# Optimization experiments

Measured on AMD Instinct MI355X. Metric: run time of the kernel, lower is better.

## Reference

```python
import jax, jax.numpy as jnp
import numpy as np

B, N, E, H = 4, 8192, 256, 8
EXP = 4  # params['num_layers'] -> MLP expansion
HID = EXP * E
EPS = 1e-5


def _layernorm(x, w, b):
    mu = jnp.mean(x, axis=-1, keepdims=True)
    var = jnp.mean(jnp.square(x - mu), axis=-1, keepdims=True)
    return (x - mu) * jax.lax.rsqrt(var + EPS) * w + b


def _mish(x):
    return x * jnp.tanh(jax.nn.softplus(x))


def setup_inputs() -> dict:
    key = jax.random.key(0)
    ks = jax.random.split(key, 12)
    s = 0.02
    return {
        "x": jax.random.normal(ks[0], (B, N, E), dtype=jnp.float32),
        "ln1_w": jnp.ones((E,), jnp.float32),
        "ln1_b": jnp.zeros((E,), jnp.float32),
        "Wq": jax.random.normal(ks[1], (E, E), jnp.float32) * s,
        "bq": jnp.zeros((E,), jnp.float32),
        "Wk": jax.random.normal(ks[2], (E, E), jnp.float32) * s,
        "bk": jnp.zeros((E,), jnp.float32),
        "Wv": jax.random.normal(ks[3], (E, E), jnp.float32) * s,
        "bv": jnp.zeros((E,), jnp.float32),
        "Wp": jax.random.normal(ks[4], (E, E), jnp.float32) * s,
        "bp": jnp.zeros((E,), jnp.float32),
        "ln2_w": jnp.ones((E,), jnp.float32),
        "ln2_b": jnp.zeros((E,), jnp.float32),
        "W1": jax.random.normal(ks[5], (HID, E), jnp.float32) * s,
        "b1": jnp.zeros((HID,), jnp.float32),
        "W2": jax.random.normal(ks[6], (E, HID), jnp.float32) * s,
        "b2": jnp.zeros((E,), jnp.float32),
    }


def _msa(x, Wq, bq, Wk, bk, Wv, bv, Wp, bp):
    b, n, e = x.shape
    d = n // H  # sequence-chunk per head (faithful to source rearrange)
    q = (x @ Wq.T + bq).reshape(b, H, d, e)
    k = (x @ Wk.T + bk).reshape(b, H, d, e)
    v = (x @ Wv.T + bv).reshape(b, H, d, e)
    scale = jnp.sqrt(jnp.float32(E))
    energy = jnp.einsum('bhie,bhke->bhik', q, k)  # (b,H,d,d)
    att = jax.nn.softmax(energy, axis=3) / scale
    o = jnp.einsum('bhik,bhke->bhie', att, v).reshape(b, n, e)
    return o @ Wp.T + bp


def reference(x, ln1_w, ln1_b, Wq, bq, Wk, bk, Wv, bv, Wp, bp,
              ln2_w, ln2_b, W1, b1, W2, b2):
    # pre-LN attention block + residual
    x1 = _msa(_layernorm(x, ln1_w, ln1_b), Wq, bq, Wk, bk, Wv, bv, Wp, bp) + x
    # pre-LN MLP (Mish after both linears, per source) + residual
    h = _layernorm(x1, ln2_w, ln2_b)
    h = _mish(h @ W1.T + b1)
    h = _mish(h @ W2.T + b2)
    return h + x1
```

## Files before the change

kernel.cpp:

```cpp
#include <hip/hip_runtime.h>

typedef float  f32x4  __attribute__((ext_vector_type(4)));
typedef float  f4v    __attribute__((ext_vector_type(4)));
typedef __bf16 bf16x8 __attribute__((ext_vector_type(8)));
typedef __bf16 bf16x4 __attribute__((ext_vector_type(4)));
typedef unsigned short ushort_t;

#define AS1 __attribute__((address_space(1)))
#define AS3 __attribute__((address_space(3)))

static __device__ __forceinline__ void gload_lds16(const void* g, void* l) {
  __builtin_amdgcn_global_load_lds((const AS1 void*)g, (AS3 void*)l, 16, 0, 0);
}

static __device__ __forceinline__ float mishf(float x) {
  float t = __expf(x);
  float u = t * (t + 2.f);
  float y = x * __fdividef(u, u + 2.f);
  return (x > 15.f) ? x : y;
}

__global__ __launch_bounds__(256) void packw(
    const float* __restrict__ Wq, const float* __restrict__ Wk,
    const float* __restrict__ Wv, const float* __restrict__ Wp,
    const float* __restrict__ W1, const float* __restrict__ W2,
    __bf16* __restrict__ out)
{
  const int t = blockIdx.x * 256 + threadIdx.x;
  const int e0 = t * 8;
  int rel, K; const float* src;
  if      (e0 < 196608) { rel = e0;          K = 256;  src = nullptr; }
  else if (e0 < 262144) { rel = e0 - 196608; K = 256;  src = Wp; }
  else if (e0 < 524288) { rel = e0 - 262144; K = 256;  src = W1; }
  else                  { rel = e0 - 524288; K = 1024; src = W2; }
  const int percb = (K >> 8) * 8192;
  const int cb = rel / percb;  const int r1 = rel % percb;
  const int c  = r1 / 8192;    const int r2 = r1 % 8192;
  const int u  = r2 / 1024;    const int r3 = r2 % 1024;
  const int n  = r3 / 512;     const int l  = (r3 % 512) >> 3;
  const int col = cb * 32 + n * 16 + (l & 15);
  const int k   = c * 256 + u * 32 + ((l >> 4) << 3);
  const float* sp;
  if (e0 < 196608) {
    const float* qkvsrc = (col < 256) ? Wq : (col < 512 ? Wk : Wv);
    sp = qkvsrc + (size_t)(col & 255) * 256 + k;
  } else {
    sp = src + (size_t)col * K + k;
  }
  const f4v a = *(const f4v*)(sp);
  const f4v b = *(const f4v*)(sp + 4);
  bf16x8 o;
  #pragma unroll
  for (int j = 0; j < 4; ++j) { o[j] = (__bf16)a[j]; o[4 + j] = (__bf16)b[j]; }
  *(bf16x8*)(out + e0) = o;
}

__global__ void packb(const float* __restrict__ a, const float* __restrict__ b,
                      const float* __restrict__ c, float* __restrict__ o) {
  int i = threadIdx.x;
  o[i] = (i < 256) ? a[i] : (i < 512 ? b[i - 256] : c[i - 512]);
}

__global__ __launch_bounds__(256) void ln_rows(
    const float* __restrict__ X, const float* __restrict__ g,
    const float* __restrict__ b, __bf16* __restrict__ Y)
{
  const int l = threadIdx.x & 63;
  const size_t row = (size_t)blockIdx.x * 4 + (threadIdx.x >> 6);
  const f4v x = *(const f4v*)(X + row * 256 + l * 4);
  float s = x[0] + x[1] + x[2] + x[3];
  float q = x[0]*x[0] + x[1]*x[1] + x[2]*x[2] + x[3]*x[3];
  #pragma unroll
  for (int d = 1; d < 64; d <<= 1) { s += __shfl_xor(s, d); q += __shfl_xor(q, d); }
  const float mu = s * (1.f / 256.f);
  const float rs = rsqrtf(q * (1.f / 256.f) - mu * mu + 1e-5f);
  const f4v gv = *(const f4v*)(g + l * 4);
  const f4v bv = *(const f4v*)(b + l * 4);
  bf16x4 o;
  #pragma unroll
  for (int j = 0; j < 4; ++j) o[j] = (__bf16)((x[j] - mu) * rs * gv[j] + bv[j]);
  *(bf16x4*)(Y + row * 256 + l * 4) = o;
}

template<int BM, int NT, int KC, int ACT, int RES, int OUTBF>
__global__ __launch_bounds__(512, 2) void bgemm(
    const __bf16* __restrict__ A, const __bf16* __restrict__ Wg,
    const float* __restrict__ bias, const float* __restrict__ res,
    void* __restrict__ out, int ldo)
{
  constexpr int K  = KC * 256;
  constexpr int MR = BM / 16;
  __shared__ __bf16 Ab[BM * 256];
  const int tid = threadIdx.x, l = tid & 63, w = tid >> 6;
  constexpr int nwg = (32768 / BM) * NT;
  const int wg = (blockIdx.x & 7) * (nwg / 8) + (blockIdx.x >> 3);
  const int mt = wg / NT, nt = wg % NT;
  const int row0 = mt * BM;
  const int col0 = nt * 256 + w * 32;
  const int cb = nt * 8 + w;

  auto stageA = [&](int c) {
    #pragma unroll
    for (int j = 0; j < BM / 16; ++j) {
      const int s = j * 512 + tid;
      const int r = s >> 5, q = s & 31;
      gload_lds16(A + (size_t)(row0 + r) * K + c * 256 + ((q ^ (r & 7)) << 3),
                  &Ab[s << 3]);
    }
  };

  bf16x8 bf[2][8];
  auto loadB = [&](int c) {
    const __bf16* wp = Wg + (size_t)(cb * KC + c) * 8192;
    #pragma unroll
    for (int u = 0; u < 8; ++u)
      #pragma unroll
      for (int n = 0; n < 2; ++n)
        bf[n][u] = *(const bf16x8*)(wp + (((u << 1) | n) * 64 + l) * 8);
  };

  f32x4 acc[MR][2] = {};

  stageA(0); loadB(0);
  asm volatile("s_waitcnt vmcnt(0)" ::: "memory");
  __builtin_amdgcn_s_barrier();

  for (int c = 0;;) {
    #pragma unroll
    for (int u = 0; u < 8; ++u) {
      bf16x8 af[MR];
      #pragma unroll
      for (int m = 0; m < MR; ++m) {
        const int r = m * 16 + (l & 15);
        const int q = ((u << 2) | (l >> 4)) ^ (r & 7);
        af[m] = *(const bf16x8*)&Ab[((r << 5) | q) << 3];
      }
      #pragma unroll
      for (int m = 0; m < MR; ++m) {
        acc[m][0] = __builtin_amdgcn_mfma_f32_16x16x32_bf16(af[m], bf[0][u], acc[m][0], 0, 0, 0);
        acc[m][1] = __builtin_amdgcn_mfma_f32_16x16x32_bf16(af[m], bf[1][u], acc[m][1], 0, 0, 0);
      }
    }
    if (++c == KC) break;
    __syncthreads();
    stageA(c);
    loadB(c);
    asm volatile("s_waitcnt vmcnt(0)" ::: "memory");
    __builtin_amdgcn_s_barrier();
  }

  const float b0 = bias[col0 + (l & 15)];
  const float b1 = bias[col0 + 16 + (l & 15)];
  #pragma unroll
  for (int m = 0; m < MR; ++m) {
    #pragma unroll
    for (int r = 0; r < 4; ++r) {
      const int row = row0 + m * 16 + ((l >> 4) << 2) + r;
      float v0 = acc[m][0][r] + b0;
      float v1 = acc[m][1][r] + b1;
      if (ACT) { v0 = mishf(v0); v1 = mishf(v1); }
      if (OUTBF) {
        __bf16* op = (__bf16*)out + (size_t)row * ldo + col0;
        op[l & 15]        = (__bf16)v0;
        op[16 + (l & 15)] = (__bf16)v1;
      } else {
        if (RES) {
          const float* rp = res + (size_t)row * ldo + col0;
          v0 += rp[l & 15];
          v1 += rp[16 + (l & 15)];
        }
        float* op = (float*)out + (size_t)row * ldo + col0;
        op[l & 15]        = v0;
        op[16 + (l & 15)] = v1;
      }
    }
  }
}

__global__ __launch_bounds__(512) void attn_fwd(
    const __bf16* __restrict__ QKV, __bf16* __restrict__ Om)
{
  __shared__ __bf16 Ks[2][32][256];
  __shared__ __bf16 Vs[2][256][32];
  __shared__ __bf16 Ps[8][16][32];
  const int tid = threadIdx.x, l = tid & 63, w = tid >> 6;
  const int wgs = (blockIdx.x & 7) * 32 + (blockIdx.x >> 3);
  const int bh = wgs >> 3, qt = wgs & 7;
  const size_t rbase = (size_t)bh * 1024 * 768;
  const int qr0 = qt * 128 + w * 16;

  bf16x8 qf[8];
  {
    const __bf16* qp = QKV + rbase + (size_t)(qr0 + (l & 15)) * 768 + ((l >> 4) << 3);
    #pragma unroll
    for (int s = 0; s < 8; ++s) qf[s] = *(const bf16x8*)(qp + s * 32);
  }
  f32x4 acc[16] = {};
  float lacc[4] = {0.f, 0.f, 0.f, 0.f};

  const int kec = tid & 31, kr_ = tid >> 5;
  const int vp = tid & 15, vc = tid >> 4;
  const __bf16* gK = QKV + 256 + rbase + kec * 8;
  const __bf16* gV = QKV + 512 + rbase + vc * 8;

  uint4 rk0, rk1, rv0, rv1;
  auto ldKV = [&](int kt) {
    const __bf16* k0 = gK + (size_t)(kt * 32 + kr_) * 768;
    rk0 = *(const uint4*)k0;
    rk1 = *(const uint4*)(k0 + 16 * 768);
    const __bf16* v0 = gV + (size_t)(kt * 32 + vp * 2) * 768;
    rv0 = *(const uint4*)v0;
    rv1 = *(const uint4*)(v0 + 768);
  };
  auto wrKV = [&](int buf) {
    char* kb = (char*)&Ks[buf][0][0];
    const int a0 = (kr_ * 512 + kec * 16) ^ ((kr_ & 15) << 4);
    const int a1 = ((kr_ + 16) * 512 + kec * 16) ^ (((kr_ + 16) & 15) << 4);
    *(uint4*)(kb + a0) = rk0;
    *(uint4*)(kb + a1) = rk1;
    const ushort_t* s0 = (const ushort_t*)&rv0;
    const ushort_t* s1 = (const ushort_t*)&rv1;
    #pragma unroll
    for (int i = 0; i < 8; ++i) {
      unsigned pk = (unsigned)s0[i] | ((unsigned)s1[i] << 16);
      *(unsigned*)&Vs[buf][vc * 8 + i][vp * 2] = pk;
    }
  };

  ldKV(0); wrKV(0);
  __syncthreads();
  int cur = 0;
  for (int kt = 0;;) {
    if (kt + 1 < 32) ldKV(kt + 1);
    f32x4 S[2] = {};
    const char* kbase = (const char*)&Ks[cur][0][0];
    #pragma unroll
    for (int t = 0; t < 2; ++t) {
      const int kcol = t * 16 + (l & 15);
      const int swz = (kcol & 15) << 4;
      #pragma unroll
      for (int s = 0; s < 8; ++s) {
        uint4 kf = *(const uint4*)(kbase + ((kcol * 512 + s * 64 + ((l >> 4) << 4)) ^ swz));
        S[t] = __builtin_amdgcn_mfma_f32_16x16x32_bf16(qf[s], __builtin_bit_cast(bf16x8, kf), S[t], 0, 0, 0);
      }
    }
    #pragma unroll
    for (int t = 0; t < 2; ++t)
      #pragma unroll
      for (int r = 0; r < 4; ++r) {
        float p = __expf(S[t][r]);
        lacc[r] += p;
        Ps[w][((l >> 4) << 2) + r][t * 16 + (l & 15)] = (__bf16)p;
      }
    bf16x8 pf = *(const bf16x8*)&Ps[w][l & 15][(l >> 4) << 3];
    #pragma unroll
    for (int n = 0; n < 16; ++n) {
      uint4 vf = *(const uint4*)&Vs[cur][n * 16 + (l & 15)][(l >> 4) << 3];
      acc[n] = __builtin_amdgcn_mfma_f32_16x16x32_bf16(pf, __builtin_bit_cast(bf16x8, vf), acc[n], 0, 0, 0);
    }
    if (++kt == 32) break;
    wrKV(cur ^ 1);
    __syncthreads();
    cur ^= 1;
  }
  f32x4 inv;
  #pragma unroll
  for (int r = 0; r < 4; ++r) {
    float s = lacc[r];
    s += __shfl_xor(s, 1); s += __shfl_xor(s, 2);
    s += __shfl_xor(s, 4); s += __shfl_xor(s, 8);
    inv[r] = 1.f / (16.f * s);
  }
  __bf16* op = Om + (size_t)(bh * 1024 + qr0 + ((l >> 4) << 2)) * 256 + (l & 15);
  #pragma unroll
  for (int n = 0; n < 16; ++n)
    #pragma unroll
    for (int r = 0; r < 4; ++r)
      op[(size_t)r * 256 + n * 16] = (__bf16)(acc[n][r] * inv[r]);
}

extern "C" void kernel_launch(void* const* d_in, const int* in_sizes, int n_in,
                              void* d_out, int out_size, void* d_ws, size_t ws_size,
                              hipStream_t stream)
{
  const float* x    = (const float*)d_in[0];
  const float* ln1w = (const float*)d_in[1];
  const float* ln1b = (const float*)d_in[2];
  const float* Wq   = (const float*)d_in[3];
  const float* bq   = (const float*)d_in[4];
  const float* Wk   = (const float*)d_in[5];
  const float* bk   = (const float*)d_in[6];
  const float* Wv   = (const float*)d_in[7];
  const float* bv   = (const float*)d_in[8];
  const float* Wp   = (const float*)d_in[9];
  const float* bp   = (const float*)d_in[10];
  const float* ln2w = (const float*)d_in[11];
  const float* ln2b = (const float*)d_in[12];
  const float* W1   = (const float*)d_in[13];
  const float* b1   = (const float*)d_in[14];
  const float* W2   = (const float*)d_in[15];
  const float* b2   = (const float*)d_in[16];

  char* ws = (char*)d_ws;
  __bf16* wb   = (__bf16*)(ws);
  float*  bqkv = (float*)(ws + 1572864);
  __bf16* y    = (__bf16*)(ws + 2097152);
  __bf16* qkv  = (__bf16*)(ws + 18874368);
  float*  x1   = (float*)(ws + 18874368);
  __bf16* hb   = (__bf16*)(ws + 52428800);
  __bf16* h1   = (__bf16*)(ws + 69206016);
  __bf16* ao   = y;
  float*  outp = (float*)d_out;

  packw<<<384, 256, 0, stream>>>(Wq, Wk, Wv, Wp, W1, W2, wb);
  packb<<<1, 768, 0, stream>>>(bq, bk, bv, bqkv);
  ln_rows<<<8192, 256, 0, stream>>>(x, ln1w, ln1b, y);
  bgemm<128, 3, 1, 0, 0, 1><<<768,  512, 0, stream>>>(y,  wb,          bqkv, nullptr, qkv,  768);
  attn_fwd<<<256, 512, 0, stream>>>(qkv, ao);
  bgemm<64, 1, 1, 0, 1, 0><<<512,  512, 0, stream>>>(ao, wb + 196608, bp,   x,       x1,   256);
  ln_rows<<<8192, 256, 0, stream>>>(x1, ln2w, ln2b, hb);
  bgemm<128, 4, 1, 1, 0, 1><<<1024, 512, 0, stream>>>(hb, wb + 262144, b1,  nullptr, h1,  1024);
  bgemm<64, 1, 4, 1, 1, 0><<<512,  512, 0, stream>>>(h1, wb + 524288, b2,   x1,      outp, 256);
}
```

Before: 214.8 us.

## Swizzle attention V/P shared tiles and stream GEMM B fragments per k-step

In the attention kernel the V and P shared-memory tiles get an XOR swizzle on 16-byte chunks, applied to both writes and reads, to cut LDS bank conflicts on the packed V stores and the P/V fragment loads. In the GEMM kernel the B weight fragments are no longer preloaded for a whole K chunk (16 vector registers). They are double-buffered one k-step ahead inside the MFMA loop. This lowers register pressure and overlaps global B loads with compute, but adds global-load latency inside the inner loop.

```diff
diff --git a/kernel.cpp b/kernel.cpp
--- a/kernel.cpp
+++ b/kernel.cpp
@@ -109,25 +109,25 @@
     }
   };
 
-  bf16x8 bf[2][8];
-  auto loadB = [&](int c) {
-    const __bf16* wp = Wg + (size_t)(cb * KC + c) * 8192;
-    #pragma unroll
-    for (int u = 0; u < 8; ++u)
-      #pragma unroll
-      for (int n = 0; n < 2; ++n)
-        bf[n][u] = *(const bf16x8*)(wp + (((u << 1) | n) * 64 + l) * 8);
+  auto ldBu = [&](bf16x8* d, int c, int u) {
+    const __bf16* wp = Wg + (size_t)(cb * KC + c) * 8192 + (((u << 1) * 64 + l) << 3);
+    d[0] = *(const bf16x8*)(wp);
+    d[1] = *(const bf16x8*)(wp + 512);
   };
 
   f32x4 acc[MR][2] = {};
 
-  stageA(0); loadB(0);
+  stageA(0);
   asm volatile("s_waitcnt vmcnt(0)" ::: "memory");
   __builtin_amdgcn_s_barrier();
 
   for (int c = 0;;) {
+    bf16x8 b0[2], b1[2];
+    ldBu(b0, c, 0);
     #pragma unroll
     for (int u = 0; u < 8; ++u) {
+      if (u + 1 < 8) ldBu((u & 1) ? b0 : b1, c, u + 1);
+      const bf16x8* bu = (u & 1) ? b1 : b0;
       bf16x8 af[MR];
       #pragma unroll
       for (int m = 0; m < MR; ++m) {
@@ -137,27 +137,26 @@
       }
       #pragma unroll
       for (int m = 0; m < MR; ++m) {
-        acc[m][0] = __builtin_amdgcn_mfma_f32_16x16x32_bf16(af[m], bf[0][u], acc[m][0], 0, 0, 0);
-        acc[m][1] = __builtin_amdgcn_mfma_f32_16x16x32_bf16(af[m], bf[1][u], acc[m][1], 0, 0, 0);
+        acc[m][0] = __builtin_amdgcn_mfma_f32_16x16x32_bf16(af[m], bu[0], acc[m][0], 0, 0, 0);
+        acc[m][1] = __builtin_amdgcn_mfma_f32_16x16x32_bf16(af[m], bu[1], acc[m][1], 0, 0, 0);
       }
     }
     if (++c == KC) break;
     __syncthreads();
     stageA(c);
-    loadB(c);
     asm volatile("s_waitcnt vmcnt(0)" ::: "memory");
     __builtin_amdgcn_s_barrier();
   }
 
-  const float b0 = bias[col0 + (l & 15)];
-  const float b1 = bias[col0 + 16 + (l & 15)];
+  const float b0s = bias[col0 + (l & 15)];
+  const float b1s = bias[col0 + 16 + (l & 15)];
   #pragma unroll
   for (int m = 0; m < MR; ++m) {
     #pragma unroll
     for (int r = 0; r < 4; ++r) {
       const int row = row0 + m * 16 + ((l >> 4) << 2) + r;
-      float v0 = acc[m][0][r] + b0;
-      float v1 = acc[m][1][r] + b1;
+      float v0 = acc[m][0][r] + b0s;
+      float v1 = acc[m][1][r] + b1s;
       if (ACT) { v0 = mishf(v0); v1 = mishf(v1); }
       if (OUTBF) {
         __bf16* op = (__bf16*)out + (size_t)row * ldo + col0;
@@ -181,8 +180,8 @@
     const __bf16* __restrict__ QKV, __bf16* __restrict__ Om)
 {
   __shared__ __bf16 Ks[2][32][256];
-  __shared__ __bf16 Vs[2][256][32];
-  __shared__ __bf16 Ps[8][16][32];
+  __shared__ __bf16 Vs[2][256 * 32];
+  __shared__ __bf16 Ps[8][16 * 32];
   const int tid = threadIdx.x, l = tid & 63, w = tid >> 6;
   const int wgs = (blockIdx.x & 7) * 32 + (blockIdx.x >> 3);
   const int bh = wgs >> 3, qt = wgs & 7;
@@ -218,12 +217,16 @@
     const int a1 = ((kr_ + 16) * 512 + kec * 16) ^ (((kr_ + 16) & 15) << 4);
     *(uint4*)(kb + a0) = rk0;
     *(uint4*)(kb + a1) = rk1;
+    char* vb = (char*)&Vs[buf][0];
     const ushort_t* s0 = (const ushort_t*)&rv0;
     const ushort_t* s1 = (const ushort_t*)&rv1;
+    const int u = vp >> 2, ub = (vp & 3) * 4;
     #pragma unroll
     for (int i = 0; i < 8; ++i) {
       unsigned pk = (unsigned)s0[i] | ((unsigned)s1[i] << 16);
-      *(unsigned*)&Vs[buf][vc * 8 + i][vp * 2] = pk;
+      const int row = vc * 8 + i;
+      const int swz = u ^ (row & 3) ^ ((row >> 3) & 3);
+      *(unsigned*)(vb + row * 64 + (swz << 4) + ub) = pk;
     }
   };
 
@@ -244,18 +247,27 @@
         S[t] = __builtin_amdgcn_mfma_f32_16x16x32_bf16(qf[s], __builtin_bit_cast(bf16x8, kf), S[t], 0, 0, 0);
       }
     }
+    char* pb = (char*)&Ps[w][0];
     #pragma unroll
     for (int t = 0; t < 2; ++t)
       #pragma unroll
       for (int r = 0; r < 4; ++r) {
         float p = __expf(S[t][r]);
         lacc[r] += p;
-        Ps[w][((l >> 4) << 2) + r][t * 16 + (l & 15)] = (__bf16)p;
-      }
-    bf16x8 pf = *(const bf16x8*)&Ps[w][l & 15][(l >> 4) << 3];
+        const int qr = ((l >> 4) << 2) + r;
+        const int c = t * 16 + (l & 15);
+        const int swz = (c >> 3) ^ (qr & 3) ^ ((qr >> 2) & 3);
+        *(__bf16*)(pb + qr * 64 + (swz << 4) + ((c & 7) * 2)) = (__bf16)p;
+      }
+    const int prow = l & 15;
+    const int pswz = (l >> 4) ^ (prow & 3) ^ ((prow >> 2) & 3);
+    bf16x8 pf = *(const bf16x8*)(pb + prow * 64 + (pswz << 4));
+    const char* vb = (const char*)&Vs[cur][0];
     #pragma unroll
     for (int n = 0; n < 16; ++n) {
-      uint4 vf = *(const uint4*)&Vs[cur][n * 16 + (l & 15)][(l >> 4) << 3];
+      const int row = n * 16 + (l & 15);
+      const int swz = (l >> 4) ^ (row & 3) ^ ((row >> 3) & 3);
+      uint4 vf = *(const uint4*)(vb + row * 64 + (swz << 4));
       acc[n] = __builtin_amdgcn_mfma_f32_16x16x32_bf16(pf, __builtin_bit_cast(bf16x8, vf), acc[n], 0, 0, 0);
     }
     if (++kt == 32) break;
```

After: 203.9 us. 1.05x faster.

## Use 2x4 wave tiling in bgemm and stream B fragments per k-step

Applied to the files above, without the earlier changes.

The GEMM's 8 waves are rearranged from a 1x8 column layout (each wave covering all BM rows and 32 columns) to a 2x4 layout where each wave covers half the rows and 64 columns. This halves the A-fragment LDS reads per MFMA. B-fragment registers are no longer preloaded for a whole 256-wide K chunk; they are double-buffered per k-step, loading step u+1 while step u computes. The aim is less LDS traffic and fewer held registers, which should help occupancy. The cost is that B global loads now sit inside the inner loop, where their latency may not be fully hidden.

```diff
diff --git a/kernel.cpp b/kernel.cpp
--- a/kernel.cpp
+++ b/kernel.cpp
@@ -89,15 +89,16 @@
     void* __restrict__ out, int ldo)
 {
   constexpr int K  = KC * 256;
-  constexpr int MR = BM / 16;
+  constexpr int MR = BM / 32;
   __shared__ __bf16 Ab[BM * 256];
   const int tid = threadIdx.x, l = tid & 63, w = tid >> 6;
+  const int wr = w >> 2, wc = w & 3;
   constexpr int nwg = (32768 / BM) * NT;
   const int wg = (blockIdx.x & 7) * (nwg / 8) + (blockIdx.x >> 3);
   const int mt = wg / NT, nt = wg % NT;
   const int row0 = mt * BM;
-  const int col0 = nt * 256 + w * 32;
-  const int cb = nt * 8 + w;
+  const int col0 = nt * 256 + wc * 64;
+  const int cb0 = nt * 8 + wc * 2;
 
   auto stageA = [&](int c) {
     #pragma unroll
@@ -109,69 +110,75 @@
     }
   };
 
-  bf16x8 bf[2][8];
-  auto loadB = [&](int c) {
-    const __bf16* wp = Wg + (size_t)(cb * KC + c) * 8192;
-    #pragma unroll
-    for (int u = 0; u < 8; ++u)
-      #pragma unroll
-      for (int n = 0; n < 2; ++n)
-        bf[n][u] = *(const bf16x8*)(wp + (((u << 1) | n) * 64 + l) * 8);
+  auto ldBu = [&](bf16x8* d, int c, int u) {
+    const __bf16* wp0 = Wg + ((size_t)cb0 * KC + c) * 8192 + (((u << 1) * 64 + l) << 3);
+    const __bf16* wp1 = wp0 + (size_t)KC * 8192;
+    d[0] = *(const bf16x8*)(wp0);
+    d[1] = *(const bf16x8*)(wp0 + 512);
+    d[2] = *(const bf16x8*)(wp1);
+    d[3] = *(const bf16x8*)(wp1 + 512);
   };
 
-  f32x4 acc[MR][2] = {};
-
-  stageA(0); loadB(0);
+  f32x4 acc[MR][4] = {};
+
+  stageA(0);
   asm volatile("s_waitcnt vmcnt(0)" ::: "memory");
   __builtin_amdgcn_s_barrier();
 
   for (int c = 0;;) {
+    bf16x8 b0[4], b1[4];
+    ldBu(b0, c, 0);
     #pragma unroll
     for (int u = 0; u < 8; ++u) {
+      if (u + 1 < 8) ldBu((u & 1) ? b0 : b1, c, u + 1);
+      const bf16x8* bu = (u & 1) ? b1 : b0;
       bf16x8 af[MR];
       #pragma unroll
       for (int m = 0; m < MR; ++m) {
-        const int r = m * 16 + (l & 15);
+        const int r = wr * (BM / 2) + m * 16 + (l & 15);
         const int q = ((u << 2) | (l >> 4)) ^ (r & 7);
         af[m] = *(const bf16x8*)&Ab[((r << 5) | q) << 3];
       }
       #pragma unroll
-      for (int m = 0; m < MR; ++m) {
-        acc[m][0] = __builtin_amdgcn_mfma_f32_16x16x32_bf16(af[m], bf[0][u], acc[m][0], 0, 0, 0);
-        acc[m][1] = __builtin_amdgcn_mfma_f32_16x16x32_bf16(af[m], bf[1][u], acc[m][1], 0, 0, 0);
-      }
+      for (int m = 0; m < MR; ++m)
+        #pragma unroll
+        for (int n = 0; n < 4; ++n)
+          acc[m][n] = __builtin_amdgcn_mfma_f32_16x16x32_bf16(af[m], bu[n], acc[m][n], 0, 0, 0);
     }
     if (++c == KC) break;
     __syncthreads();
     stageA(c);
-    loadB(c);
     asm volatile("s_waitcnt vmcnt(0)" ::: "memory");
     __builtin_amdgcn_s_barrier();
   }
 
-  const float b0 = bias[col0 + (l & 15)];
-  const float b1 = bias[col0 + 16 + (l & 15)];
+  float bs[4];
+  #pragma unroll
+  for (int n = 0; n < 4; ++n) bs[n] = bias[col0 + n * 16 + (l & 15)];
   #pragma unroll
   for (int m = 0; m < MR; ++m) {
     #pragma unroll
     for (int r = 0; r < 4; ++r) {
-      const int row = row0 + m * 16 + ((l >> 4) << 2) + r;
-      float v0 = acc[m][0][r] + b0;
-      float v1 = acc[m][1][r] + b1;
-      if (ACT) { v0 = mishf(v0); v1 = mishf(v1); }
+      const int row = row0 + wr * (BM / 2) + m * 16 + ((l >> 4) << 2) + r;
+      float v[4];
+      #pragma unroll
+      for (int n = 0; n < 4; ++n) {
+        v[n] = acc[m][n][r] + bs[n];
+        if (ACT) v[n] = mishf(v[n]);
+      }
       if (OUTBF) {
         __bf16* op = (__bf16*)out + (size_t)row * ldo + col0;
-        op[l & 15]        = (__bf16)v0;
-        op[16 + (l & 15)] = (__bf16)v1;
+        #pragma unroll
+        for (int n = 0; n < 4; ++n) op[n * 16 + (l & 15)] = (__bf16)v[n];
       } else {
+        float* op = (float*)out + (size_t)row * ldo + col0;
         if (RES) {
           const float* rp = res + (size_t)row * ldo + col0;
-          v0 += rp[l & 15];
-          v1 += rp[16 + (l & 15)];
+          #pragma unroll
+          for (int n = 0; n < 4; ++n) v[n] += rp[n * 16 + (l & 15)];
         }
-        float* op = (float*)out + (size_t)row * ldo + col0;
-        op[l & 15]        = v0;
-        op[16 + (l & 15)] = v1;
+        #pragma unroll
+        for (int n = 0; n < 4; ++n) op[n * 16 + (l & 15)] = v[n];
       }
     }
   }
```

Measured after the change: 204.0 us. -5.0%, faster.
